# Performance work log

Measured on AMD Instinct MI355X. Metric: run time of the kernel, lower is better.

The kernel has to match this reference:

```python
import jax, jax.numpy as jnp
import numpy as np

T, B, INPUT, LATENT = 256, 128, 1024, 2048


def setup_inputs() -> dict:
    key = jax.random.key(0)
    k1, k2, k3, k4, k5 = jax.random.split(key, 5)
    s_i = 1.0 / np.sqrt(INPUT)
    s_h = 1.0 / np.sqrt(LATENT)
    return {
        "x": jax.random.normal(k1, (T, B, INPUT), dtype=jnp.float32),
        "W_i": jax.random.uniform(k2, (LATENT, INPUT), jnp.float32, -s_i, s_i),
        "b_i": jax.random.uniform(k3, (LATENT,), jnp.float32, -s_i, s_i),
        "W_h": jax.random.uniform(k4, (LATENT, LATENT), jnp.float32, -s_h, s_h),
        "b_h": jax.random.uniform(k5, (LATENT,), jnp.float32, -s_h, s_h),
    }


def reference(x, W_i, b_i, W_h, b_h):
    # Precompute the input projection for all timesteps in one big GEMM:
    # [T, B, INPUT] @ [INPUT, LATENT] -> [T, B, LATENT]
    xi = jnp.einsum("tbi,li->tbl", x, W_i) + b_i
    # Step 0: h = None in torch -> tanh(W_i x) only (no W_h term, no b_h).
    h0 = jnp.tanh(xi[0])

    def step(h, xi_t):
        h_new = jnp.tanh(xi_t + h @ W_h.T + b_h)
        return h_new, h_new

    _, hs = jax.lax.scan(step, h0, xi[1:])
    # [T, B, LATENT]
    return jnp.concatenate([h0[None], hs], axis=0)
```

## Files before the change

### kernel.cpp

```cpp
#include <hip/hip_runtime.h>
#include <hip/hip_bf16.h>
#include <math.h>

#define T_STEPS 256
#define BATCH   128
#define IN_DIM  1024
#define LAT     2048

#define NG      8
#define GB      32
#define GROWS   16
#define GCOLS   64

typedef __bf16 bf16x8 __attribute__((ext_vector_type(8)));
typedef __bf16 bf16x4 __attribute__((ext_vector_type(4)));
typedef float  f32x4  __attribute__((ext_vector_type(4)));
typedef float  f32x2  __attribute__((ext_vector_type(2)));

#define MFMA16 __builtin_amdgcn_mfma_f32_16x16x32_bf16

__device__ __forceinline__ void coh_store32(__bf16* p, unsigned int v) {
    __hip_atomic_store((unsigned int*)p, v,
                       __ATOMIC_RELAXED, __HIP_MEMORY_SCOPE_AGENT);
}
__device__ __forceinline__ unsigned int pack_bf16(float a, float b) {
    union { __bf16 h[2]; unsigned int u; } p;
    p.h[0] = (__bf16)a; p.h[1] = (__bf16)b;
    return p.u;
}
__device__ __forceinline__ unsigned int coh_poll_u32(const unsigned int* p) {
    unsigned int v;
    asm volatile("global_load_dword %0, %1, off sc1" : "=v"(v) : "v"(p) : "memory");
    asm volatile("s_waitcnt vmcnt(0)" ::: "memory");
    return v;
}
__device__ __forceinline__ void coh_store_flag(unsigned int* p) {
    unsigned int one = 1;
    asm volatile("global_store_dword %0, %1, off sc1"
                 :: "v"(p), "v"(one) : "memory");
}

__device__ __forceinline__ int swz(int row, int kbyte) {
    return (row * 64 + kbyte) ^ ((row & 7) << 4);
}

template<int ROWS>
__device__ __forceinline__ void stage_load(const float* __restrict__ src, int ld,
                                           int tid, f32x4* regs) {
#pragma unroll
    for (int rnd = 0; rnd < ROWS / 32; ++rnd) {
        int r  = rnd * 32 + (tid >> 3);
        int kc = (tid & 7) * 4;
        regs[rnd] = *(const f32x4*)(src + (size_t)r * ld + kc);
    }
}

template<int ROWS>
__device__ __forceinline__ void stage_write(const f32x4* regs, char* hi, char* lo,
                                            int tid) {
#pragma unroll
    for (int rnd = 0; rnd < ROWS / 32; ++rnd) {
        int r  = rnd * 32 + (tid >> 3);
        int kc = (tid & 7) * 4;
        bf16x4 vh, vl;
        f32x4  v = regs[rnd];
#pragma unroll
        for (int e = 0; e < 4; ++e) {
            float x = v[e];
            __bf16 h = (__bf16)x;
            vh[e] = h;
            vl[e] = (__bf16)(x - (float)h);
        }
        int off = swz(r, kc * 2);
        *(bf16x4*)(hi + off) = vh;
        *(bf16x4*)(lo + off) = vl;
    }
}

__device__ __forceinline__ bf16x8 ld_frag(const char* p, int row, int kb) {
    return *(const bf16x8*)(p + swz(row, kb));
}

__device__ __forceinline__ void split8(f32x4 v0, f32x4 v1, bf16x8& hi, bf16x8& lo) {
#pragma unroll
    for (int e = 0; e < 4; ++e) {
        __bf16 h0 = (__bf16)v0[e];
        hi[e]     = h0;
        lo[e]     = (__bf16)(v0[e] - (float)h0);
        __bf16 h1 = (__bf16)v1[e];
        hi[e + 4] = h1;
        lo[e + 4] = (__bf16)(v1[e] - (float)h1);
    }
}

__global__ __launch_bounds__(256)
void k_prep(const float* __restrict__ W, __bf16* __restrict__ hi)
{
    size_t i = ((size_t)blockIdx.x * 256 + threadIdx.x) * 4;
    f32x4 v = *(const f32x4*)(W + i);
    bf16x4 vh;
#pragma unroll
    for (int e = 0; e < 4; ++e) vh[e] = (__bf16)v[e];
    *(bf16x4*)(hi + i) = vh;
}

__global__ __launch_bounds__(256, 2)
void k_xproj(const float* __restrict__ x, const float* __restrict__ Wi,
             const float* __restrict__ bi, float* __restrict__ out,
             __bf16* __restrict__ h0hi)
{
    __shared__ __align__(16) char lds[32 * 1024];
    char* Ahi = lds;
    char* Alo = lds + 8192;
    char* Bhi = lds + 16384;
    char* Blo = lds + 24576;

    int tid  = threadIdx.x;
    int lane = tid & 63;
    int w    = tid >> 6;
    int wm   = (w >> 1) * 64;
    int wn   = (w & 1) * 64;
    int bm   = blockIdx.y * 128;
    int bn   = blockIdx.x * 128;

    const float* Abase = x  + (size_t)bm * IN_DIM;
    const float* Bbase = Wi + (size_t)bn * IN_DIM;

    f32x4 acc[4][4] = {};
    f32x4 ra[4], rb[4];

    stage_load<128>(Abase, IN_DIM, tid, ra);
    stage_load<128>(Bbase, IN_DIM, tid, rb);

    for (int k0 = 0; k0 < IN_DIM; k0 += 32) {
        stage_write<128>(ra, Ahi, Alo, tid);
        stage_write<128>(rb, Bhi, Blo, tid);
        __syncthreads();

        if (k0 + 32 < IN_DIM) {
            stage_load<128>(Abase + k0 + 32, IN_DIM, tid, ra);
            stage_load<128>(Bbase + k0 + 32, IN_DIM, tid, rb);
        }

        int kb = (lane >> 4) * 16;
        bf16x8 ah[4], al[4], bh[4], bl[4];
#pragma unroll
        for (int i = 0; i < 4; ++i) {
            int rrow = i * 16 + (lane & 15);
            ah[i] = ld_frag(Ahi, wm + rrow, kb);
            al[i] = ld_frag(Alo, wm + rrow, kb);
            bh[i] = ld_frag(Bhi, wn + rrow, kb);
            bl[i] = ld_frag(Blo, wn + rrow, kb);
        }
#pragma unroll
        for (int i = 0; i < 4; ++i)
#pragma unroll
            for (int j = 0; j < 4; ++j) {
                acc[i][j] = MFMA16(ah[i], bh[j], acc[i][j], 0, 0, 0);
                acc[i][j] = MFMA16(ah[i], bl[j], acc[i][j], 0, 0, 0);
                acc[i][j] = MFMA16(al[i], bh[j], acc[i][j], 0, 0, 0);
            }
        __syncthreads();
    }

#pragma unroll
    for (int j = 0; j < 4; ++j) {
        int n = bn + wn + j * 16 + (lane & 15);
        float bias = bi[n];
#pragma unroll
        for (int i = 0; i < 4; ++i) {
            int m0 = bm + wm + i * 16 + ((lane >> 4) * 4);
#pragma unroll
            for (int r = 0; r < 4; ++r) {
                float v = acc[i][j][r] + bias;
                if (m0 + r < BATCH) {
                    v = tanhf(v);
                    if (h0hi)
                        h0hi[(size_t)(m0 + r) * LAT + n] = (__bf16)v;
                }
                out[(size_t)(m0 + r) * LAT + n] = v;
            }
        }
    }
}

#define LOADA(dst, off)                                                       \
    asm volatile("global_load_dwordx4 %0, %1, off offset:" #off " sc1"        \
                 : "=v"(dst) : "v"(Ar) : "memory")

#define LOADB(dst, base, off)                                                 \
    asm volatile("global_load_dwordx4 %0, %1, off offset:" #off               \
                 : "=v"(dst) : "v"(base))

__global__ __launch_bounds__(512, 2)
void k_recur(const __bf16* __restrict__ Whi,
             __bf16* __restrict__ p0h, __bf16* __restrict__ p1h,
             const float* __restrict__ bias, float* __restrict__ out,
             unsigned int* __restrict__ flags)
{
    __shared__ __align__(16) float part[8][GROWS][GCOLS + 2];

    const int tid  = threadIdx.x;
    const int lane = tid & 63;
    const int w    = tid >> 6;

    const int bid = blockIdx.x;
    const int rg  = bid >> 5;
    const int cb  = bid & 31;
    const int bm  = rg * GROWS;
    const int bn  = cb * GCOLS;

    const int fr    = lane & 15;
    const int kq    = (lane >> 4) * 8;
    const int kbase = w * 256 + kq;

    bf16x8 bq[4][8];
    {
        const __bf16* B0 = Whi + (size_t)(bn + fr) * LAT + kbase;
        const __bf16* B1 = B0 + (size_t)16 * LAT;
        const __bf16* B2 = B0 + (size_t)32 * LAT;
        const __bf16* B3 = B0 + (size_t)48 * LAT;
        LOADB(bq[0][0], B0,   0); LOADB(bq[0][1], B0,  64);
        LOADB(bq[0][2], B0, 128); LOADB(bq[0][3], B0, 192);
        LOADB(bq[0][4], B0, 256); LOADB(bq[0][5], B0, 320);
        LOADB(bq[0][6], B0, 384); LOADB(bq[0][7], B0, 448);
        LOADB(bq[1][0], B1,   0); LOADB(bq[1][1], B1,  64);
        LOADB(bq[1][2], B1, 128); LOADB(bq[1][3], B1, 192);
        LOADB(bq[1][4], B1, 256); LOADB(bq[1][5], B1, 320);
        LOADB(bq[1][6], B1, 384); LOADB(bq[1][7], B1, 448);
        LOADB(bq[2][0], B2,   0); LOADB(bq[2][1], B2,  64);
        LOADB(bq[2][2], B2, 128); LOADB(bq[2][3], B2, 192);
        LOADB(bq[2][4], B2, 256); LOADB(bq[2][5], B2, 320);
        LOADB(bq[2][6], B2, 384); LOADB(bq[2][7], B2, 448);
        LOADB(bq[3][0], B3,   0); LOADB(bq[3][1], B3,  64);
        LOADB(bq[3][2], B3, 128); LOADB(bq[3][3], B3, 192);
        LOADB(bq[3][4], B3, 256); LOADB(bq[3][5], B3, 320);
        LOADB(bq[3][6], B3, 384); LOADB(bq[3][7], B3, 448);
        asm volatile("s_waitcnt vmcnt(0)" ::: "memory");
        __builtin_amdgcn_sched_barrier(0);
    }

    const int    orow = tid >> 5;
    const int    oc   = (tid & 31) * 2;
    const size_t idx  = (size_t)(bm + orow) * LAT + bn + oc;
    const float  bv0  = bias[bn + oc];
    const float  bv1  = bias[bn + oc + 1];

    const __bf16* Ah = p0h;
    __bf16*       Nh = p1h;

    f32x2 xv = *(const f32x2*)(out + (size_t)1 * (BATCH * LAT) + idx);

    for (int t = 1; t < T_STEPS; ++t) {
        float* io = out + (size_t)t * (BATCH * LAT);

        if (t > 1) {
            const unsigned int* fp =
                flags + ((size_t)(t - 1) * NG + rg) * GB + w * 4;
            for (;;) {
                unsigned int f = 1;
                if (lane < 4) f = coh_poll_u32(fp + lane);
                if (__all(f != 0)) break;
                __builtin_amdgcn_s_sleep(2);
            }
        }

        const __bf16* Ar = Ah + (size_t)(bm + fr) * LAT + kbase;

        bf16x8 a[8];
        LOADA(a[0],   0);
        LOADA(a[1],  64);
        LOADA(a[2], 128);
        LOADA(a[3], 192);
        LOADA(a[4], 256);
        LOADA(a[5], 320);
        LOADA(a[6], 384);
        LOADA(a[7], 448);
        asm volatile("s_waitcnt vmcnt(0)" ::: "memory");
        __builtin_amdgcn_sched_barrier(0);

        f32x4 acc[4] = {};
#pragma unroll
        for (int i = 0; i < 8; ++i)
#pragma unroll
            for (int cf = 0; cf < 4; ++cf)
                acc[cf] = MFMA16(a[i], bq[cf][i], acc[cf], 0, 0, 0);

        f32x2 xn = {};
        if (t + 1 < T_STEPS)
            xn = *(const f32x2*)(out + (size_t)(t + 1) * (BATCH * LAT) + idx);

#pragma unroll
        for (int cf = 0; cf < 4; ++cf)
#pragma unroll
            for (int r = 0; r < 4; ++r)
                part[w][(lane >> 4) * 4 + r][cf * 16 + fr] = acc[cf][r];

        __syncthreads();

        float s0 = 0.f, s1 = 0.f;
#pragma unroll
        for (int p = 0; p < 8; ++p) {
            f32x2 v = *(const f32x2*)&part[p][orow][oc];
            s0 += v[0];
            s1 += v[1];
        }

        float o0 = tanhf(s0 + bv0 + xv[0]);
        float o1 = tanhf(s1 + bv1 + xv[1]);

        coh_store32(Nh + idx, pack_bf16(o0, o1));

        asm volatile("s_waitcnt vmcnt(0)" ::: "memory");
        __syncthreads();
        if (tid == 0 && t + 1 < T_STEPS)
            coh_store_flag(flags + ((size_t)t * NG + rg) * GB + cb);

        f32x2 ov; ov[0] = o0; ov[1] = o1;
        *(f32x2*)(io + idx) = ov;

        xv = xn;
        __bf16* tmp = (__bf16*)Ah; Ah = Nh; Nh = tmp;
    }
}

__global__ __launch_bounds__(256, 2)
void k_step_f32(const float* __restrict__ hprev, const float* __restrict__ Wh,
                const float* __restrict__ bias, float* __restrict__ io)
{
    __shared__ __align__(16) float part[4][32][32];

    const int tid  = threadIdx.x;
    const int lane = tid & 63;
    const int w    = tid >> 6;

    const int id  = blockIdx.x;
    const int j_  = id >> 3;
    const int bn  = ((id & 7) * 8 + (j_ >> 2)) * 32;
    const int bm  = (j_ & 3) * 32;

    const int fr = lane & 15;
    const int kq = (lane >> 4) * 8;

    const float* A0 = hprev + (size_t)(bm + fr)      * LAT;
    const float* A1 = hprev + (size_t)(bm + 16 + fr) * LAT;
    const float* B0 = Wh    + (size_t)(bn + fr)      * LAT;
    const float* B1 = Wh    + (size_t)(bn + 16 + fr) * LAT;

    f32x4 acc[2][2] = {};
    const int kbase = w * 512 + kq;
#pragma unroll
    for (int i = 0; i < 16; ++i) {
        const int k = kbase + i * 32;
        f32x4 a00 = *(const f32x4*)(A0 + k);
        f32x4 a01 = *(const f32x4*)(A0 + k + 4);
        f32x4 a10 = *(const f32x4*)(A1 + k);
        f32x4 a11 = *(const f32x4*)(A1 + k + 4);
        f32x4 b00 = *(const f32x4*)(B0 + k);
        f32x4 b01 = *(const f32x4*)(B0 + k + 4);
        f32x4 b10 = *(const f32x4*)(B1 + k);
        f32x4 b11 = *(const f32x4*)(B1 + k + 4);

        bf16x8 ah0, al0, ah1, al1, bh0, bl0, bh1, bl1;
        split8(a00, a01, ah0, al0);
        split8(a10, a11, ah1, al1);
        split8(b00, b01, bh0, bl0);
        split8(b10, b11, bh1, bl1);

        acc[0][0] = MFMA16(ah0, bh0, acc[0][0], 0, 0, 0);
        acc[0][1] = MFMA16(ah0, bh1, acc[0][1], 0, 0, 0);
        acc[1][0] = MFMA16(ah1, bh0, acc[1][0], 0, 0, 0);
        acc[1][1] = MFMA16(ah1, bh1, acc[1][1], 0, 0, 0);
        acc[0][0] = MFMA16(al0, bh0, acc[0][0], 0, 0, 0);
        acc[0][1] = MFMA16(al0, bh1, acc[0][1], 0, 0, 0);
        acc[1][0] = MFMA16(al1, bh0, acc[1][0], 0, 0, 0);
        acc[1][1] = MFMA16(al1, bh1, acc[1][1], 0, 0, 0);
        acc[0][0] = MFMA16(ah0, bl0, acc[0][0], 0, 0, 0);
        acc[0][1] = MFMA16(ah0, bl1, acc[0][1], 0, 0, 0);
        acc[1][0] = MFMA16(ah1, bl0, acc[1][0], 0, 0, 0);
        acc[1][1] = MFMA16(ah1, bl1, acc[1][1], 0, 0, 0);
    }

#pragma unroll
    for (int mi = 0; mi < 2; ++mi)
#pragma unroll
        for (int nj = 0; nj < 2; ++nj)
#pragma unroll
            for (int r = 0; r < 4; ++r)
                part[w][mi * 16 + (lane >> 4) * 4 + r][nj * 16 + fr] = acc[mi][nj][r];

    __syncthreads();

    const int row = tid >> 3;
    const int c   = (tid & 7) * 4;
    f32x4 s0 = *(const f32x4*)&part[0][row][c];
    f32x4 s1 = *(const f32x4*)&part[1][row][c];
    f32x4 s2 = *(const f32x4*)&part[2][row][c];
    f32x4 s3 = *(const f32x4*)&part[3][row][c];

    float* outp = io + (size_t)(bm + row) * LAT + bn + c;
    f32x4 xv = *(const f32x4*)outp;
    f32x4 bv = *(const f32x4*)(bias + bn + c);
    f32x4 o;
#pragma unroll
    for (int e = 0; e < 4; ++e)
        o[e] = tanhf(s0[e] + s1[e] + s2[e] + s3[e] + xv[e] + bv[e]);
    *(f32x4*)outp = o;
}

extern "C" void kernel_launch(void* const* d_in, const int* in_sizes, int n_in,
                              void* d_out, int out_size, void* d_ws, size_t ws_size,
                              hipStream_t stream) {
    const float* x  = (const float*)d_in[0];
    const float* Wi = (const float*)d_in[1];
    const float* bi = (const float*)d_in[2];
    const float* Wh = (const float*)d_in[3];
    const float* bh = (const float*)d_in[4];
    float* out = (float*)d_out;

    const size_t whbytes = (size_t)LAT * LAT * 2;
    const size_t hbytes  = (size_t)BATCH * LAT * 2;
    const size_t fbytes  = (size_t)T_STEPS * NG * GB * sizeof(unsigned int);
    const size_t need    = whbytes + 2 * hbytes + fbytes;
    const bool fast = ws_size >= need;

    char* wsb = (char*)d_ws;
    __bf16* Whi = (__bf16*)wsb;
    __bf16* p0h = (__bf16*)(wsb + whbytes);
    __bf16* p1h = (__bf16*)(wsb + whbytes + hbytes);
    unsigned int* flags = (unsigned int*)(wsb + whbytes + 2 * hbytes);

    if (fast) {
        hipMemsetAsync(flags, 0, fbytes, stream);
        k_prep<<<(LAT * LAT) / (256 * 4), 256, 0, stream>>>(Wh, Whi);
    }

    dim3 g1(LAT / 128, (T_STEPS * BATCH) / 128);
    k_xproj<<<g1, 256, 0, stream>>>(x, Wi, bi, out, fast ? p0h : nullptr);

    if (fast) {
        k_recur<<<NG * GB, 512, 0, stream>>>(Whi, p0h, p1h, bh, out, flags);
    } else {
        for (int t = 1; t < T_STEPS; ++t)
            k_step_f32<<<256, 256, 0, stream>>>(out + (size_t)(t - 1) * BATCH * LAT,
                                                Wh, bh,
                                                out + (size_t)t * BATCH * LAT);
    }
}
```

Baseline: 1.703 ms.

## Use per-timestep hidden-state planes so recurrent loads can use cached plain loads

Adds a mode where each timestep writes its bf16 hidden state to its own workspace plane. Because no address is ever rewritten, readers can use ordinary cacheable vector loads instead of sc1 coherent loads; the old two-buffer ping-pong path is kept as a fallback when the workspace is too small. It also changes the block-to-tile mapping so the row group comes from the low bits of the block id, and shortens the poll sleep. The new mode needs about 256 times more workspace for hidden states. Correctness relies on each plane being written exactly once per call and on no stale copies of it sitting in non-coherent caches.

```diff
diff --git a/kernel.cpp b/kernel.cpp
--- a/kernel.cpp
+++ b/kernel.cpp
@@ -6,6 +6,7 @@
 #define BATCH   128
 #define IN_DIM  1024
 #define LAT     2048
+#define NBLK    256
 
 #define NG      8
 #define GB      32
@@ -19,25 +20,19 @@
 
 #define MFMA16 __builtin_amdgcn_mfma_f32_16x16x32_bf16
 
-__device__ __forceinline__ void coh_store32(__bf16* p, unsigned int v) {
-    __hip_atomic_store((unsigned int*)p, v,
-                       __ATOMIC_RELAXED, __HIP_MEMORY_SCOPE_AGENT);
+__device__ __forceinline__ unsigned int poll_sc1(const unsigned int* p) {
+    unsigned int v;
+    asm volatile("global_load_dword %0, %1, off sc1" : "=v"(v) : "v"(p) : "memory");
+    asm volatile("s_waitcnt vmcnt(0)" ::: "memory");
+    return v;
+}
+__device__ __forceinline__ void st_sc1(unsigned int* p, unsigned int v) {
+    asm volatile("global_store_dword %0, %1, off sc1" :: "v"(p), "v"(v) : "memory");
 }
 __device__ __forceinline__ unsigned int pack_bf16(float a, float b) {
     union { __bf16 h[2]; unsigned int u; } p;
     p.h[0] = (__bf16)a; p.h[1] = (__bf16)b;
     return p.u;
-}
-__device__ __forceinline__ unsigned int coh_poll_u32(const unsigned int* p) {
-    unsigned int v;
-    asm volatile("global_load_dword %0, %1, off sc1" : "=v"(v) : "v"(p) : "memory");
-    asm volatile("s_waitcnt vmcnt(0)" ::: "memory");
-    return v;
-}
-__device__ __forceinline__ void coh_store_flag(unsigned int* p) {
-    unsigned int one = 1;
-    asm volatile("global_store_dword %0, %1, off sc1"
-                 :: "v"(p), "v"(one) : "memory");
 }
 
 __device__ __forceinline__ int swz(int row, int kbyte) {
@@ -184,35 +179,26 @@
     }
 }
 
-#define LOADA(dst, off)                                                       \
+#define LOADA_S(dst, base, off)                                               \
     asm volatile("global_load_dwordx4 %0, %1, off offset:" #off " sc1"        \
-                 : "=v"(dst) : "v"(Ar) : "memory")
+                 : "=v"(dst) : "v"(base) : "memory")
 
 #define LOADB(dst, base, off)                                                 \
     asm volatile("global_load_dwordx4 %0, %1, off offset:" #off               \
                  : "=v"(dst) : "v"(base))
 
-__global__ __launch_bounds__(512, 2)
-void k_recur(const __bf16* __restrict__ Whi,
-             __bf16* __restrict__ p0h, __bf16* __restrict__ p1h,
-             const float* __restrict__ bias, float* __restrict__ out,
-             unsigned int* __restrict__ flags)
+template<bool FRESH>
+__device__ __forceinline__ void recur_body(
+    const __bf16* __restrict__ Whi, __bf16* __restrict__ hpl,
+    const float* __restrict__ bias, float* __restrict__ out,
+    unsigned int* __restrict__ flags,
+    float (&part)[8][GROWS][GCOLS + 2],
+    int tid, int lane, int w, int rg, int cb, int bm, int bn)
 {
-    __shared__ __align__(16) float part[8][GROWS][GCOLS + 2];
-
-    const int tid  = threadIdx.x;
-    const int lane = tid & 63;
-    const int w    = tid >> 6;
-
-    const int bid = blockIdx.x;
-    const int rg  = bid >> 5;
-    const int cb  = bid & 31;
-    const int bm  = rg * GROWS;
-    const int bn  = cb * GCOLS;
-
     const int fr    = lane & 15;
     const int kq    = (lane >> 4) * 8;
     const int kbase = w * 256 + kq;
+    const size_t HN = (size_t)BATCH * LAT;
 
     bf16x8 bq[4][8];
     {
@@ -246,9 +232,6 @@
     const float  bv0  = bias[bn + oc];
     const float  bv1  = bias[bn + oc + 1];
 
-    const __bf16* Ah = p0h;
-    __bf16*       Nh = p1h;
-
     f32x2 xv = *(const f32x2*)(out + (size_t)1 * (BATCH * LAT) + idx);
 
     for (int t = 1; t < T_STEPS; ++t) {
@@ -259,25 +242,29 @@
                 flags + ((size_t)(t - 1) * NG + rg) * GB + w * 4;
             for (;;) {
                 unsigned int f = 1;
-                if (lane < 4) f = coh_poll_u32(fp + lane);
+                if (lane < 4) f = poll_sc1(fp + lane);
                 if (__all(f != 0)) break;
-                __builtin_amdgcn_s_sleep(2);
+                __builtin_amdgcn_s_sleep(1);
             }
         }
 
-        const __bf16* Ar = Ah + (size_t)(bm + fr) * LAT + kbase;
+        const __bf16* Aplane = FRESH ? hpl + HN * (size_t)(t - 1)
+                                     : hpl + HN * (size_t)((t - 1) & 1);
+        const __bf16* Ar = Aplane + (size_t)(bm + fr) * LAT + kbase;
 
         bf16x8 a[8];
-        LOADA(a[0],   0);
-        LOADA(a[1],  64);
-        LOADA(a[2], 128);
-        LOADA(a[3], 192);
-        LOADA(a[4], 256);
-        LOADA(a[5], 320);
-        LOADA(a[6], 384);
-        LOADA(a[7], 448);
-        asm volatile("s_waitcnt vmcnt(0)" ::: "memory");
-        __builtin_amdgcn_sched_barrier(0);
+        if constexpr (FRESH) {
+#pragma unroll
+            for (int i = 0; i < 8; ++i)
+                a[i] = *(const bf16x8*)(Ar + i * 32);
+        } else {
+            LOADA_S(a[0], Ar,   0); LOADA_S(a[1], Ar,  64);
+            LOADA_S(a[2], Ar, 128); LOADA_S(a[3], Ar, 192);
+            LOADA_S(a[4], Ar, 256); LOADA_S(a[5], Ar, 320);
+            LOADA_S(a[6], Ar, 384); LOADA_S(a[7], Ar, 448);
+            asm volatile("s_waitcnt vmcnt(0)" ::: "memory");
+            __builtin_amdgcn_sched_barrier(0);
+        }
 
         f32x4 acc[4] = {};
 #pragma unroll
@@ -309,19 +296,42 @@
         float o0 = tanhf(s0 + bv0 + xv[0]);
         float o1 = tanhf(s1 + bv1 + xv[1]);
 
-        coh_store32(Nh + idx, pack_bf16(o0, o1));
+        __bf16* Np = FRESH ? hpl + HN * (size_t)t
+                           : hpl + HN * (size_t)(t & 1);
+        st_sc1((unsigned int*)(Np + idx), pack_bf16(o0, o1));
 
         asm volatile("s_waitcnt vmcnt(0)" ::: "memory");
         __syncthreads();
         if (tid == 0 && t + 1 < T_STEPS)
-            coh_store_flag(flags + ((size_t)t * NG + rg) * GB + cb);
+            st_sc1(flags + ((size_t)t * NG + rg) * GB + cb, 1u);
 
         f32x2 ov; ov[0] = o0; ov[1] = o1;
         *(f32x2*)(io + idx) = ov;
 
         xv = xn;
-        __bf16* tmp = (__bf16*)Ah; Ah = Nh; Nh = tmp;
-    }
+    }
+}
+
+template<bool FRESH>
+__global__ __launch_bounds__(512, 2)
+void k_recur(const __bf16* __restrict__ Whi, __bf16* __restrict__ hpl,
+             const float* __restrict__ bias, float* __restrict__ out,
+             unsigned int* __restrict__ flags)
+{
+    __shared__ __align__(16) float part[8][GROWS][GCOLS + 2];
+
+    const int tid  = threadIdx.x;
+    const int lane = tid & 63;
+    const int w    = tid >> 6;
+
+    const int bid = blockIdx.x;
+    const int rg  = bid & 7;
+    const int cb  = bid >> 3;
+    const int bm  = rg * GROWS;
+    const int bn  = cb * GCOLS;
+
+    recur_body<FRESH>(Whi, hpl, bias, out, flags, part,
+                      tid, lane, w, rg, cb, bm, bn);
 }
 
 __global__ __launch_bounds__(256, 2)
@@ -421,25 +431,32 @@
     const size_t whbytes = (size_t)LAT * LAT * 2;
     const size_t hbytes  = (size_t)BATCH * LAT * 2;
     const size_t fbytes  = (size_t)T_STEPS * NG * GB * sizeof(unsigned int);
-    const size_t need    = whbytes + 2 * hbytes + fbytes;
-    const bool fast = ws_size >= need;
+
+    const size_t need_fresh = whbytes + (size_t)T_STEPS * hbytes + fbytes;
+    const size_t need_pp    = whbytes + 2 * hbytes + fbytes;
+
+    const bool fresh = ws_size >= need_fresh;
+    const bool pp    = !fresh && ws_size >= need_pp;
 
     char* wsb = (char*)d_ws;
     __bf16* Whi = (__bf16*)wsb;
-    __bf16* p0h = (__bf16*)(wsb + whbytes);
-    __bf16* p1h = (__bf16*)(wsb + whbytes + hbytes);
-    unsigned int* flags = (unsigned int*)(wsb + whbytes + 2 * hbytes);
-
-    if (fast) {
+    __bf16* hpl = (__bf16*)(wsb + whbytes);
+    const size_t nplanes = fresh ? T_STEPS : 2;
+    unsigned int* flags = (unsigned int*)(wsb + whbytes + nplanes * hbytes);
+
+    if (fresh || pp) {
         hipMemsetAsync(flags, 0, fbytes, stream);
         k_prep<<<(LAT * LAT) / (256 * 4), 256, 0, stream>>>(Wh, Whi);
     }
 
     dim3 g1(LAT / 128, (T_STEPS * BATCH) / 128);
-    k_xproj<<<g1, 256, 0, stream>>>(x, Wi, bi, out, fast ? p0h : nullptr);
-
-    if (fast) {
-        k_recur<<<NG * GB, 512, 0, stream>>>(Whi, p0h, p1h, bh, out, flags);
+    k_xproj<<<g1, 256, 0, stream>>>(x, Wi, bi, out,
+                                    (fresh || pp) ? hpl : nullptr);
+
+    if (fresh) {
+        k_recur<true ><<<NBLK, 512, 0, stream>>>(Whi, hpl, bh, out, flags);
+    } else if (pp) {
+        k_recur<false><<<NBLK, 512, 0, stream>>>(Whi, hpl, bh, out, flags);
     } else {
         for (int t = 1; t < T_STEPS; ++t)
             k_step_f32<<<256, 256, 0, stream>>>(out + (size_t)(t - 1) * BATCH * LAT,
```

After: 1.420 ms. 1.2x faster.
